# Optimization experiments

Measured on AMD Instinct MI355X. Metric: run time of the kernel, lower is better.

## Reference

```python
import jax, jax.numpy as jnp
import numpy as np

D_MODEL = 1024
NUM_HEADS = 16
HEAD_DIM = D_MODEL // NUM_HEADS


def setup_inputs() -> dict:
    key = jax.random.key(0)
    ks = jax.random.split(key, 9)
    s = 1.0 / np.sqrt(D_MODEL)
    return {
        "x": jax.random.normal(ks[0], (4, 2048, D_MODEL), dtype=jnp.float32),
        "Wq": jax.random.uniform(ks[1], (D_MODEL, D_MODEL), minval=-s, maxval=s, dtype=jnp.float32),
        "bq": jax.random.uniform(ks[2], (D_MODEL,), minval=-s, maxval=s, dtype=jnp.float32),
        "Wk": jax.random.uniform(ks[3], (D_MODEL, D_MODEL), minval=-s, maxval=s, dtype=jnp.float32),
        "bk": jax.random.uniform(ks[4], (D_MODEL,), minval=-s, maxval=s, dtype=jnp.float32),
        "Wv": jax.random.uniform(ks[5], (D_MODEL, D_MODEL), minval=-s, maxval=s, dtype=jnp.float32),
        "bv": jax.random.uniform(ks[6], (D_MODEL,), minval=-s, maxval=s, dtype=jnp.float32),
        "Wo": jax.random.uniform(ks[7], (D_MODEL, D_MODEL), minval=-s, maxval=s, dtype=jnp.float32),
        "bo": jax.random.uniform(ks[8], (D_MODEL,), minval=-s, maxval=s, dtype=jnp.float32),
    }


def reference(x, Wq, bq, Wk, bk, Wv, bv, Wo, bo):
    B, T, C = x.shape
    H, Dh = NUM_HEADS, HEAD_DIM
    # projections (nn.Linear applies x @ W^T + b)
    q = (x @ Wq.T + bq).reshape(B, T, H, Dh).transpose(0, 2, 1, 3)  # [B,H,T,Dh]
    k = (x @ Wk.T + bk).reshape(B, T, H, Dh).transpose(0, 2, 1, 3)
    v = (x @ Wv.T + bv).reshape(B, T, H, Dh).transpose(0, 2, 1, 3)
    scale = 1.0 / np.sqrt(Dh).astype(np.float32)
    att = jnp.einsum("bhqd,bhkd->bhqk", q, k) * scale  # [B,H,T,T]
    causal = jnp.tril(jnp.ones((T, T), dtype=bool))
    att = jnp.where(causal[None, None], att, -jnp.inf)
    att = jax.nn.softmax(att, axis=-1)
    # dropout is identity in eval mode
    out = jnp.einsum("bhqk,bhkd->bhqd", att, v)  # [B,H,T,Dh]
    out = out.transpose(0, 2, 1, 3).reshape(B, T, C)
    return out @ Wo.T + bo
```

## Files before the change

kernel.cpp:

```cpp
#include <hip/hip_runtime.h>
#include <stdint.h>

typedef __attribute__((ext_vector_type(8))) short short8;
typedef __attribute__((ext_vector_type(4))) short short4v;
typedef __attribute__((ext_vector_type(4))) float floatx4;
typedef __attribute__((ext_vector_type(16))) float floatx16;

#define QSCALE 0.1803368801111f

__device__ __forceinline__ unsigned short f2bf(float f) {
  unsigned int u = __float_as_uint(f);
  unsigned int r = (u + 0x7FFFu + ((u >> 16) & 1u)) >> 16;
  return (unsigned short)r;
}

__device__ __forceinline__ unsigned int cvt_pk_bf16(float lo, float hi) {
  unsigned int r;
  asm("v_cvt_pk_bf16_f32 %0, %1, %2" : "=v"(r) : "v"(lo), "v"(hi));
  return r;
}

__device__ __forceinline__ float max3f(float a, float b, float c) {
  float r;
  asm("v_max3_f32 %0, %1, %2, %3" : "=v"(r) : "v"(a), "v"(b), "v"(c));
  return r;
}

__device__ __forceinline__ void async_copy16(void* lds, const void* g) {
  __builtin_amdgcn_global_load_lds(
      (const __attribute__((address_space(1))) unsigned int*)g,
      (__attribute__((address_space(3))) unsigned int*)lds, 16, 0, 0);
}

__global__ __launch_bounds__(256) void f2ball_kernel(
    const float* __restrict__ x, unsigned short* __restrict__ xb,
    const float* __restrict__ w0, const float* __restrict__ w1,
    const float* __restrict__ w2, const float* __restrict__ w3,
    unsigned short* __restrict__ o0, unsigned short* __restrict__ o1,
    unsigned short* __restrict__ o2, unsigned short* __restrict__ o3) {
  const float* in;
  unsigned short* out;
  long i;
  if (blockIdx.x < 8192) {
    in = x;
    out = xb;
    i = (long)blockIdx.x * 256 + threadIdx.x;
  } else {
    int wb = blockIdx.x - 8192;
    int which = wb >> 10;
    in = (which == 0) ? w0 : (which == 1) ? w1 : (which == 2) ? w2 : w3;
    out = (which == 0) ? o0 : (which == 1) ? o1 : (which == 2) ? o2 : o3;
    i = (long)(wb & 1023) * 256 + threadIdx.x;
  }
  float4 v = ((const float4*)in)[i];
  short4v o;
  o[0] = (short)f2bf(v.x);
  o[1] = (short)f2bf(v.y);
  o[2] = (short)f2bf(v.z);
  o[3] = (short)f2bf(v.w);
  *(short4v*)(out + i * 4) = o;
}

__device__ __forceinline__ void gemm128_mainloop_db(
    const unsigned short* __restrict__ A, const unsigned short* __restrict__ Bt,
    int K, long brow, long bcol, unsigned short* As, unsigned short* Bs,
    floatx4 acc[4][4]) {
  const int tid = threadIdx.x;
  const int wave = tid >> 6;
  const int lane = tid & 63;
  const int wr = wave >> 1, wc = wave & 1;
  const int lr = lane & 15, lg = lane >> 4;

  const unsigned short* ga = A + (brow + (tid >> 2)) * (long)K + (tid & 3) * 8;
  const unsigned short* gb = Bt + (bcol + (tid >> 2)) * (long)K + (tid & 3) * 8;
  const int woff = wave * 512;
  const int a_off = (wr * 64 + lr) * 32 + lg * 8;
  const int b_off = (wc * 64 + lr) * 32 + lg * 8;

  async_copy16(As + woff, ga);
  async_copy16(As + woff + 2048, ga + (long)64 * K);
  async_copy16(Bs + woff, gb);
  async_copy16(Bs + woff + 2048, gb + (long)64 * K);
  ga += 32;
  gb += 32;
  __syncthreads();

  int buf = 0;
  for (int kt = 0; kt < K; kt += 32) {
    if (kt + 32 < K) {
      unsigned short* lA = As + (buf ^ 1) * 4096 + woff;
      unsigned short* lB = Bs + (buf ^ 1) * 4096 + woff;
      async_copy16(lA, ga);
      async_copy16(lA + 2048, ga + (long)64 * K);
      async_copy16(lB, gb);
      async_copy16(lB + 2048, gb + (long)64 * K);
      ga += 32;
      gb += 32;
    }
    const unsigned short* Ab = As + buf * 4096;
    const unsigned short* Bb = Bs + buf * 4096;
    short8 af[4], bf[4];
#pragma unroll
    for (int i = 0; i < 4; ++i) {
      af[i] = *(const short8*)(Ab + a_off + i * 512);
      bf[i] = *(const short8*)(Bb + b_off + i * 512);
    }
#pragma unroll
    for (int i = 0; i < 4; ++i)
#pragma unroll
      for (int j = 0; j < 4; ++j)
        acc[i][j] = __builtin_amdgcn_mfma_f32_16x16x32_bf16(af[i], bf[j], acc[i][j], 0, 0, 0);
    __syncthreads();
    buf ^= 1;
  }
}

__global__ __launch_bounds__(256, 2) void qkv_gemm256(
    const unsigned short* __restrict__ xb, const unsigned short* __restrict__ wqkv,
    const float* __restrict__ bq, const float* __restrict__ bk,
    const float* __restrict__ bv, unsigned short* __restrict__ q_out,
    unsigned short* __restrict__ k_out, unsigned short* __restrict__ vt_out) {
  __shared__ __align__(16) unsigned short Sh[24576];
  unsigned short* As = Sh;
  unsigned short* Bs = Sh + 8192;

  const int tid = threadIdx.x;
  const int wave = tid >> 6, lane = tid & 63;
  const int wr = wave >> 1, wc = wave & 1;
  const int lr = lane & 15, lg = lane >> 4;

  const long brow = (long)blockIdx.x * 128;
  const long bcol = (long)blockIdx.y * 256;

  floatx4 zero = {0.f, 0.f, 0.f, 0.f};
  floatx4 acc[4][8];
#pragma unroll
  for (int i = 0; i < 4; ++i)
#pragma unroll
    for (int j = 0; j < 8; ++j) acc[i][j] = zero;

  const int K = 1024;
  const unsigned short* ga = xb + (brow + (tid >> 2)) * (long)K + (tid & 3) * 8;
  const unsigned short* gb = wqkv + (bcol + (tid >> 2)) * (long)K + (tid & 3) * 8;
  const int woff = wave * 512;
  const int a_off = (wr * 64 + lr) * 32 + lg * 8;
  const int b_off = (wc * 128 + lr) * 32 + lg * 8;

  async_copy16(As + woff, ga);
  async_copy16(As + woff + 2048, ga + (long)64 * K);
#pragma unroll
  for (int jj = 0; jj < 4; ++jj)
    async_copy16(Bs + woff + jj * 2048, gb + (long)jj * 64 * K);
  ga += 32;
  gb += 32;
  __syncthreads();

  int buf = 0;
  for (int kt = 0; kt < K; kt += 32) {
    if (kt + 32 < K) {
      unsigned short* lA = As + (buf ^ 1) * 4096 + woff;
      unsigned short* lB = Bs + (buf ^ 1) * 8192 + woff;
      async_copy16(lA, ga);
      async_copy16(lA + 2048, ga + (long)64 * K);
#pragma unroll
      for (int jj = 0; jj < 4; ++jj)
        async_copy16(lB + jj * 2048, gb + (long)jj * 64 * K);
      ga += 32;
      gb += 32;
    }
    const unsigned short* Ab = As + buf * 4096;
    const unsigned short* Bb = Bs + buf * 8192;
    short8 av[4], bvf[8];
#pragma unroll
    for (int i = 0; i < 4; ++i) av[i] = *(const short8*)(Ab + a_off + i * 512);
#pragma unroll
    for (int j = 0; j < 8; ++j) bvf[j] = *(const short8*)(Bb + b_off + j * 512);
    __builtin_amdgcn_s_setprio(1);
#pragma unroll
    for (int i = 0; i < 4; ++i)
#pragma unroll
      for (int j = 0; j < 8; ++j)
        acc[i][j] = __builtin_amdgcn_mfma_f32_16x16x32_bf16(av[i], bvf[j], acc[i][j], 0, 0, 0);
    __builtin_amdgcn_s_setprio(0);
    __syncthreads();
    buf ^= 1;
  }

  const int kind = (int)(bcol >> 10);
  const float* bias = (kind == 0) ? bq : (kind == 1 ? bk : bv);

  if (kind == 2) {
#pragma unroll 1
    for (int half = 0; half < 2; ++half) {
      if (wc == half) {
#pragma unroll
        for (int i = 0; i < 4; ++i)
#pragma unroll
          for (int j = 0; j < 8; ++j) {
            int n_local = j * 16 + lr;
            int m_base = wr * 64 + i * 16 + lg * 4;
            float bsc = bias[(int)((bcol + half * 128 + n_local) & 1023)];
            short4v pk;
#pragma unroll
            for (int r = 0; r < 4; ++r) pk[r] = (short)f2bf(acc[i][j][r] + bsc);
            *(short4v*)(Sh + n_local * 136 + m_base) = pk;
          }
      }
      __syncthreads();
      const int b = (int)(brow >> 11);
      const int t0 = (int)(brow & 2047);
      const int f0h = (int)(bcol - 2048) + half * 128;
#pragma unroll
      for (int p = 0; p < 8; ++p) {
        int c = p * 256 + tid;
        int d_loc = c >> 4, tc = c & 15;
        short8 v = *(const short8*)(Sh + d_loc * 136 + tc * 8);
        int h = (f0h >> 6) + (d_loc >> 6);
        int d = d_loc & 63;
        *(short8*)(vt_out + ((long)((b * 16 + h) * 64 + d)) * 2048 + t0 + tc * 8) = v;
      }
      __syncthreads();
    }
  } else {
#pragma unroll
    for (int i = 0; i < 4; ++i)
#pragma unroll
      for (int j = 0; j < 8; ++j)
#pragma unroll
        for (int r = 0; r < 4; ++r) {
          int m = (int)brow + wr * 64 + i * 16 + lg * 4 + r;
          int n = (int)bcol + wc * 128 + j * 16 + lr;
          int f = n & 1023;
          float v = acc[i][j][r] + bias[f];
          if (kind == 0) v *= QSCALE;
          unsigned short o = f2bf(v);
          int h = f >> 6, d = f & 63;
          int bb = m >> 11, t = m & 2047;
          long bh = (long)(bb * 16 + h);
          if (kind == 0)
            q_out[(bh * 2048 + t) * 64 + d] = o;
          else
            k_out[(bh * 2048 + t) * 64 + d] = o;
        }
  }
}

__global__ __launch_bounds__(256, 4) void out_gemm(
    const unsigned short* __restrict__ ob, const unsigned short* __restrict__ wo,
    const float* __restrict__ bo, float* __restrict__ out) {
  __shared__ unsigned short As[2 * 128 * 32];
  __shared__ unsigned short Bs[2 * 128 * 32];
  floatx4 zero = {0.f, 0.f, 0.f, 0.f};
  floatx4 acc[4][4];
#pragma unroll
  for (int i = 0; i < 4; ++i)
#pragma unroll
    for (int j = 0; j < 4; ++j) acc[i][j] = zero;

  long brow = (long)blockIdx.x * 128;
  long bcol = (long)blockIdx.y * 128;
  gemm128_mainloop_db(ob, wo, 1024, brow, bcol, As, Bs, acc);

  const int wave = threadIdx.x >> 6, lane = threadIdx.x & 63;
  const int wr = wave >> 1, wc = wave & 1, lr = lane & 15, lg = lane >> 4;
#pragma unroll
  for (int i = 0; i < 4; ++i)
#pragma unroll
    for (int j = 0; j < 4; ++j)
#pragma unroll
      for (int r = 0; r < 4; ++r) {
        int m = (int)brow + wr * 64 + i * 16 + lg * 4 + r;
        int n = (int)bcol + wc * 64 + j * 16 + lr;
        out[(long)m * 1024 + n] = acc[i][j][r] + bo[n];
      }
}

__device__ __forceinline__ void stage_kv(char* __restrict__ Kb, char* __restrict__ Vb,
                                         const char* __restrict__ Kp,
                                         const char* __restrict__ Vt, int kv0,
                                         int tid) {
  const int wave = tid >> 6;
#pragma unroll
  for (int j = 0; j < 2; ++j) {
    int d = j * 256 + tid;
    int row = d >> 3, cc = d & 7;
    int gc = cc ^ (row & 7);
    const char* gk = Kp + (size_t)kv0 * 128 + row * 128 + gc * 16;
    async_copy16(Kb + (j * 256 + wave * 64) * 16, gk);
    const char* gv = Vt + (size_t)row * 4096 + (size_t)kv0 * 2 + gc * 16;
    async_copy16(Vb + (j * 256 + wave * 64) * 16, gv);
  }
}

__device__ __forceinline__ short8 read_frag(const char* __restrict__ base, int row,
                                            int chunk) {
  return *(const short8*)(base + row * 128 + ((chunk ^ (row & 7)) * 16));
}

__device__ __forceinline__ void attn_step(
    const char* __restrict__ Kb, const char* __restrict__ Vb,
    const short8 (&qf)[4], int kv0, int q0, int l31, int hi, bool diag,
    float& m_i, float& l_i, floatx16 (&accO)[2]) {
  floatx16 sh[2];
  __builtin_amdgcn_s_setprio(1);
#pragma unroll
  for (int hh = 0; hh < 2; ++hh) {
    floatx16 a = {0.f};
#pragma unroll
    for (int e = 1; e < 16; ++e) a[e] = 0.f;
#pragma unroll
    for (int ks = 0; ks < 4; ++ks) {
      short8 kf = read_frag(Kb, hh * 32 + l31, 2 * ks + hi);
      a = __builtin_amdgcn_mfma_f32_32x32x16_bf16(kf, qf[ks], a, 0, 0, 0);
    }
    sh[hh] = a;
  }
  __builtin_amdgcn_s_setprio(0);

  const int q = q0 + l31;
  if (diag) {
#pragma unroll
    for (int hh = 0; hh < 2; ++hh)
#pragma unroll
      for (int r = 0; r < 16; ++r) {
        int kvi = kv0 + 32 * hh + (r & 3) + 8 * (r >> 2) + 4 * hi;
        if (kvi > q) sh[hh][r] = -1e30f;
      }
  }

  float t[11];
#pragma unroll
  for (int i = 0; i < 10; ++i)
    t[i] = max3f(sh[(3 * i) / 16][(3 * i) % 16], sh[(3 * i + 1) / 16][(3 * i + 1) % 16],
                 sh[(3 * i + 2) / 16][(3 * i + 2) % 16]);
  t[10] = fmaxf(sh[1][14], sh[1][15]);
  float pmax = max3f(max3f(t[0], t[1], t[2]), max3f(t[3], t[4], t[5]),
                     max3f(t[6], t[7], t[8]));
  pmax = max3f(pmax, t[9], t[10]);

  if (__any(pmax > m_i + 11.5f)) {
    float mx = fmaxf(pmax, __shfl_xor(pmax, 32));
    float mnew = fmaxf(m_i, mx);
    float scl = exp2f(m_i - mnew);
    m_i = mnew;
    l_i *= scl;
#pragma unroll
    for (int dt = 0; dt < 2; ++dt)
#pragma unroll
      for (int r = 0; r < 16; ++r) accO[dt][r] *= scl;
  }

  float p[32];
#pragma unroll
  for (int hh = 0; hh < 2; ++hh)
#pragma unroll
    for (int r = 0; r < 16; ++r) p[hh * 16 + r] = exp2f(sh[hh][r] - m_i);
  float ls = 0.f;
#pragma unroll
  for (int i = 0; i < 8; ++i)
    ls += (p[4 * i] + p[4 * i + 1]) + (p[4 * i + 2] + p[4 * i + 3]);
  l_i += ls;

  short8 pb[4];
#pragma unroll
  for (int ks2 = 0; ks2 < 4; ++ks2) {
    const int ib = (ks2 >> 1) * 16 + (ks2 & 1) * 8;
    unsigned int a0 = cvt_pk_bf16(p[ib + 0], p[ib + 1]);
    unsigned int b0 = cvt_pk_bf16(p[ib + 4], p[ib + 5]);
    unsigned int a1 = cvt_pk_bf16(p[ib + 2], p[ib + 3]);
    unsigned int b1 = cvt_pk_bf16(p[ib + 6], p[ib + 7]);
    asm volatile("v_permlane32_swap_b32 %0, %1" : "+v"(a0), "+v"(b0));
    asm volatile("v_permlane32_swap_b32 %0, %1" : "+v"(a1), "+v"(b1));
    unsigned int w[4] = {a0, a1, b0, b1};
    pb[ks2] = *(const short8*)w;
  }

  __builtin_amdgcn_s_setprio(1);
#pragma unroll
  for (int dt = 0; dt < 2; ++dt)
#pragma unroll
    for (int ks2 = 0; ks2 < 4; ++ks2) {
      short8 vf = read_frag(Vb, dt * 32 + l31, 2 * ks2 + hi);
      accO[dt] = __builtin_amdgcn_mfma_f32_32x32x16_bf16(vf, pb[ks2], accO[dt], 0, 0, 0);
    }
  __builtin_amdgcn_s_setprio(0);
}

__global__ __launch_bounds__(256, 3) void attn_fwd(
    const unsigned short* __restrict__ qb, const unsigned short* __restrict__ kb,
    const unsigned short* __restrict__ vtb, unsigned short* __restrict__ ob) {
  __shared__ __align__(16) char Kbuf[2][8192];
  __shared__ __align__(16) char Vbuf[2][8192];

  const int id = blockIdx.x;
  const int qt = 15 - (id >> 6);
  const int bh = id & 63;

  const int tid = threadIdx.x;
  const int wave = tid >> 6, lane = tid & 63;
  const int l31 = lane & 31, hi = lane >> 5;
  const unsigned short* Q = qb + (long)bh * 2048 * 64;
  const char* Kp = (const char*)(kb + (long)bh * 2048 * 64);
  const char* Vt = (const char*)(vtb + (long)bh * 64 * 2048);
  const int b = bh >> 4, h = bh & 15;

  const int q0 = qt * 128 + wave * 32;
  const int nkv = 2 * qt + 2;

  short8 qf[4];
#pragma unroll
  for (int ks = 0; ks < 4; ++ks)
    qf[ks] = *(const short8*)(Q + (q0 + l31) * 64 + ks * 16 + hi * 8);

  floatx16 accO[2];
#pragma unroll
  for (int dt = 0; dt < 2; ++dt)
#pragma unroll
    for (int r = 0; r < 16; ++r) accO[dt][r] = 0.f;
  float m_i = -1e30f, l_i = 0.f;

  stage_kv(Kbuf[0], Vbuf[0], Kp, Vt, 0, tid);
  __syncthreads();
#pragma unroll 1
  for (int kv = 0; kv < nkv; ++kv) {
    if (kv + 1 < nkv)
      stage_kv(Kbuf[(kv + 1) & 1], Vbuf[(kv + 1) & 1], Kp, Vt, (kv + 1) * 64, tid);
    const int kv0 = kv * 64;
    if (kv0 < q0 + 32)
      attn_step(Kbuf[kv & 1], Vbuf[kv & 1], qf, kv0, q0, l31, hi,
                kv0 + 64 > q0, m_i, l_i, accO);
    __syncthreads();
  }

  float lt = l_i + __shfl_xor(l_i, 32);
  float io = 1.f / lt;
  const int q = q0 + l31;
  unsigned short* orow = ob + ((long)b * 2048 + q) * 1024 + h * 64;
#pragma unroll
  for (int dt = 0; dt < 2; ++dt)
#pragma unroll
    for (int g = 0; g < 4; ++g) {
      short4v pk;
#pragma unroll
      for (int e = 0; e < 4; ++e) pk[e] = (short)f2bf(accO[dt][4 * g + e] * io);
      *(short4v*)(orow + dt * 32 + g * 8 + hi * 4) = pk;
    }
}

extern "C" void kernel_launch(void* const* d_in, const int* in_sizes, int n_in,
                              void* d_out, int out_size, void* d_ws, size_t ws_size,
                              hipStream_t stream) {
  const float* x = (const float*)d_in[0];
  const float* bq = (const float*)d_in[2];
  const float* bk = (const float*)d_in[4];
  const float* bv = (const float*)d_in[6];
  const float* bo = (const float*)d_in[8];
  float* out = (float*)d_out;

  char* ws = (char*)d_ws;
  unsigned short* xb = (unsigned short*)(ws);
  unsigned short* wqkv = (unsigned short*)(ws + (16l << 20));
  unsigned short* wob = (unsigned short*)(ws + (22l << 20));
  unsigned short* qb = (unsigned short*)(ws + (24l << 20));
  unsigned short* kb = (unsigned short*)(ws + (40l << 20));
  unsigned short* vtb = (unsigned short*)(ws + (56l << 20));
  unsigned short* ob = (unsigned short*)(ws + (72l << 20));

  f2ball_kernel<<<12288, 256, 0, stream>>>(
      x, xb, (const float*)d_in[1], (const float*)d_in[3], (const float*)d_in[5],
      (const float*)d_in[7], wqkv, wqkv + (1l << 20), wqkv + (2l << 20), wob);

  qkv_gemm256<<<dim3(64, 12), 256, 0, stream>>>(xb, wqkv, bq, bk, bv, qb, kb, vtb);
  attn_fwd<<<1024, 256, 0, stream>>>(qb, kb, vtb, ob);
  out_gemm<<<dim3(64, 8), 256, 0, stream>>>(ob, wob, bo, out);
}
```

Measured before the change: 163.5 us.

## Split attention blocks to 64 query rows and compute row sums via MFMA

Attention blocks shrink from 4 waves covering 128 query rows to 2 waves covering 64 rows, doubling the grid. Causal work per block is then finer grained and better balanced, and diagonal blocks stop wasting K/V tile loads. The softmax row sum moves from a scalar add chain plus a cross-lane shuffle to an extra MFMA that multiplies P by a ones vector. This trades VALU work for matrix-core work and drops the final shuffle, but K/V staging is now spread over fewer threads and each tile is reloaded by twice as many blocks.

```diff
diff --git a/kernel.cpp b/kernel.cpp
--- a/kernel.cpp
+++ b/kernel.cpp
@@ -275,20 +275,20 @@
       }
 }
 
-__device__ __forceinline__ void stage_kv(char* __restrict__ Kb, char* __restrict__ Vb,
-                                         const char* __restrict__ Kp,
-                                         const char* __restrict__ Vt, int kv0,
-                                         int tid) {
+__device__ __forceinline__ void stage_kv2(char* __restrict__ Kb, char* __restrict__ Vb,
+                                          const char* __restrict__ Kp,
+                                          const char* __restrict__ Vt, int kv0,
+                                          int tid) {
   const int wave = tid >> 6;
 #pragma unroll
-  for (int j = 0; j < 2; ++j) {
-    int d = j * 256 + tid;
+  for (int j = 0; j < 4; ++j) {
+    int d = j * 128 + tid;
     int row = d >> 3, cc = d & 7;
     int gc = cc ^ (row & 7);
-    const char* gk = Kp + (size_t)kv0 * 128 + row * 128 + gc * 16;
-    async_copy16(Kb + (j * 256 + wave * 64) * 16, gk);
-    const char* gv = Vt + (size_t)row * 4096 + (size_t)kv0 * 2 + gc * 16;
-    async_copy16(Vb + (j * 256 + wave * 64) * 16, gv);
+    async_copy16(Kb + (j * 128 + wave * 64) * 16,
+                 Kp + (size_t)kv0 * 128 + row * 128 + gc * 16);
+    async_copy16(Vb + (j * 128 + wave * 64) * 16,
+                 Vt + (size_t)row * 4096 + (size_t)kv0 * 2 + gc * 16);
   }
 }
 
@@ -300,14 +300,14 @@
 __device__ __forceinline__ void attn_step(
     const char* __restrict__ Kb, const char* __restrict__ Vb,
     const short8 (&qf)[4], int kv0, int q0, int l31, int hi, bool diag,
-    float& m_i, float& l_i, floatx16 (&accO)[2]) {
+    float& m_i, floatx16& accL, floatx16 (&accO)[2]) {
   floatx16 sh[2];
   __builtin_amdgcn_s_setprio(1);
 #pragma unroll
   for (int hh = 0; hh < 2; ++hh) {
-    floatx16 a = {0.f};
-#pragma unroll
-    for (int e = 1; e < 16; ++e) a[e] = 0.f;
+    floatx16 a;
+#pragma unroll
+    for (int e = 0; e < 16; ++e) a[e] = 0.f;
 #pragma unroll
     for (int ks = 0; ks < 4; ++ks) {
       short8 kf = read_frag(Kb, hh * 32 + l31, 2 * ks + hi);
@@ -343,7 +343,7 @@
     float mnew = fmaxf(m_i, mx);
     float scl = exp2f(m_i - mnew);
     m_i = mnew;
-    l_i *= scl;
+    accL[0] *= scl;
 #pragma unroll
     for (int dt = 0; dt < 2; ++dt)
 #pragma unroll
@@ -355,11 +355,6 @@
   for (int hh = 0; hh < 2; ++hh)
 #pragma unroll
     for (int r = 0; r < 16; ++r) p[hh * 16 + r] = exp2f(sh[hh][r] - m_i);
-  float ls = 0.f;
-#pragma unroll
-  for (int i = 0; i < 8; ++i)
-    ls += (p[4 * i] + p[4 * i + 1]) + (p[4 * i + 2] + p[4 * i + 3]);
-  l_i += ls;
 
   short8 pb[4];
 #pragma unroll
@@ -375,26 +370,34 @@
     pb[ks2] = *(const short8*)w;
   }
 
+  short8 ones;
+#pragma unroll
+  for (int j = 0; j < 8; ++j) ones[j] = (short)0x3F80;
+
   __builtin_amdgcn_s_setprio(1);
 #pragma unroll
-  for (int dt = 0; dt < 2; ++dt)
-#pragma unroll
-    for (int ks2 = 0; ks2 < 4; ++ks2) {
+  for (int ks2 = 0; ks2 < 4; ++ks2) {
+#pragma unroll
+    for (int dt = 0; dt < 2; ++dt) {
       short8 vf = read_frag(Vb, dt * 32 + l31, 2 * ks2 + hi);
       accO[dt] = __builtin_amdgcn_mfma_f32_32x32x16_bf16(vf, pb[ks2], accO[dt], 0, 0, 0);
     }
+    accL = __builtin_amdgcn_mfma_f32_32x32x16_bf16(ones, pb[ks2], accL, 0, 0, 0);
+  }
   __builtin_amdgcn_s_setprio(0);
 }
 
-__global__ __launch_bounds__(256, 3) void attn_fwd(
+__global__ __launch_bounds__(128, 2) void attn_fwd(
     const unsigned short* __restrict__ qb, const unsigned short* __restrict__ kb,
     const unsigned short* __restrict__ vtb, unsigned short* __restrict__ ob) {
   __shared__ __align__(16) char Kbuf[2][8192];
   __shared__ __align__(16) char Vbuf[2][8192];
 
   const int id = blockIdx.x;
-  const int qt = 15 - (id >> 6);
-  const int bh = id & 63;
+  const int qt = 15 - (id >> 7);
+  const int r7 = id & 127;
+  const int sub = 1 - (r7 >> 6);
+  const int bh = r7 & 63;
 
   const int tid = threadIdx.x;
   const int wave = tid >> 6, lane = tid & 63;
@@ -404,8 +407,8 @@
   const char* Vt = (const char*)(vtb + (long)bh * 64 * 2048);
   const int b = bh >> 4, h = bh & 15;
 
-  const int q0 = qt * 128 + wave * 32;
-  const int nkv = 2 * qt + 2;
+  const int q0 = qt * 128 + sub * 64 + wave * 32;
+  const int nkv = 2 * qt + sub + 1;
 
   short8 qf[4];
 #pragma unroll
@@ -413,27 +416,29 @@
     qf[ks] = *(const short8*)(Q + (q0 + l31) * 64 + ks * 16 + hi * 8);
 
   floatx16 accO[2];
-#pragma unroll
-  for (int dt = 0; dt < 2; ++dt)
-#pragma unroll
-    for (int r = 0; r < 16; ++r) accO[dt][r] = 0.f;
-  float m_i = -1e30f, l_i = 0.f;
-
-  stage_kv(Kbuf[0], Vbuf[0], Kp, Vt, 0, tid);
+  floatx16 accL;
+#pragma unroll
+  for (int e = 0; e < 16; ++e) {
+    accO[0][e] = 0.f;
+    accO[1][e] = 0.f;
+    accL[e] = 0.f;
+  }
+  float m_i = -1e30f;
+
+  stage_kv2(Kbuf[0], Vbuf[0], Kp, Vt, 0, tid);
   __syncthreads();
 #pragma unroll 1
   for (int kv = 0; kv < nkv; ++kv) {
     if (kv + 1 < nkv)
-      stage_kv(Kbuf[(kv + 1) & 1], Vbuf[(kv + 1) & 1], Kp, Vt, (kv + 1) * 64, tid);
+      stage_kv2(Kbuf[(kv + 1) & 1], Vbuf[(kv + 1) & 1], Kp, Vt, (kv + 1) * 64, tid);
     const int kv0 = kv * 64;
     if (kv0 < q0 + 32)
       attn_step(Kbuf[kv & 1], Vbuf[kv & 1], qf, kv0, q0, l31, hi,
-                kv0 + 64 > q0, m_i, l_i, accO);
+                kv0 + 64 > q0, m_i, accL, accO);
     __syncthreads();
   }
 
-  float lt = l_i + __shfl_xor(l_i, 32);
-  float io = 1.f / lt;
+  float io = 1.f / accL[0];
   const int q = q0 + l31;
   unsigned short* orow = ob + ((long)b * 2048 + q) * 1024 + h * 64;
 #pragma unroll
@@ -471,6 +476,6 @@
       (const float*)d_in[7], wqkv, wqkv + (1l << 20), wqkv + (2l << 20), wob);
 
   qkv_gemm256<<<dim3(64, 12), 256, 0, stream>>>(xb, wqkv, bq, bk, bv, qb, kb, vtb);
-  attn_fwd<<<1024, 256, 0, stream>>>(qb, kb, vtb, ob);
+  attn_fwd<<<2048, 128, 0, stream>>>(qb, kb, vtb, ob);
   out_gemm<<<dim3(64, 8), 256, 0, stream>>>(ob, wob, bo, out);
 }
```

Result: slower. 179.0 us (+9.5%).
